# Optimization experiments

Measured on AMD Instinct MI355X. Metric: run time of the kernel, lower is better.

The kernel has to match this reference:

```python
import jax, jax.numpy as jnp
import numpy as np

C = 192  # in_channels
B, S, L = 4, 64, 512  # batch, spatial (patch pixels), seq_len (num patches)


def setup_inputs() -> dict:
    key = jax.random.key(0)
    ks = jax.random.split(key, 6)
    scale_in = 1.0 / np.sqrt(C)
    return {
        "query": jax.random.normal(ks[0], (B, C, S, L), jnp.float32),
        "key": jax.random.normal(ks[1], (B, C, S, L), jnp.float32),
        "value": jax.random.normal(ks[2], (B, C, S, L), jnp.float32),
        "in_proj_weight": jax.random.normal(ks[3], (1 + 2 * C, C, 1, 1), jnp.float32) * scale_in,
        "in_proj_bias": jnp.zeros((1 + 2 * C,), jnp.float32),
        "out_proj_weight": jax.random.normal(ks[4], (C, C, 1, 1), jnp.float32) * scale_in,
        "out_proj_bias": jnp.zeros((C,), jnp.float32),
    }


def reference(query, key, value, in_proj_weight, in_proj_bias, out_proj_weight, out_proj_bias):
    # Separable (linear) attention, MobileViTv2-style.
    c = query.shape[1]
    w = in_proj_weight[:, :, 0, 0]           # (1+2C, C)
    wq, wk, wv = w[:1], w[1:1 + c], w[1 + c:]
    bq, bk, bv = in_proj_bias[:1], in_proj_bias[1:1 + c], in_proj_bias[1 + c:]

    # 1x1 conv projections (pointwise GEMMs over channels)
    q = jnp.einsum('oc,bcsl->bosl', wq, query) + bq[None, :, None, None]   # (B,1,S,L)
    k = jnp.einsum('oc,bcsl->bosl', wk, key) + bk[None, :, None, None]     # (B,C,S,L)
    v = jnp.einsum('oc,bcsl->bosl', wv, value) + bv[None, :, None, None]   # (B,C,S,L)

    # Context scores: softmax over token axis (seq_len); dropout_p=0 (eval)
    context_scores = jax.nn.softmax(q, axis=-1)                            # (B,1,S,L)

    # Weighted context pooling over tokens -> global context per spatial pixel
    context = jnp.sum(k * context_scores, axis=-1, keepdims=True)          # (B,C,S,1)

    # Broadcast multiply with gated value
    out = jax.nn.relu(v) * context                                         # (B,C,S,L)

    # Out projection (1x1 conv)
    wo = out_proj_weight[:, :, 0, 0]
    out = jnp.einsum('oc,bcsl->bosl', wo, out) + out_proj_bias[None, :, None, None]
    return out
```

## Files before the change

kernel.cpp:

```cpp
#include <hip/hip_runtime.h>

#define B_ 4
#define C_ 192
#define S_ 64
#define L_ 512

typedef _Float16 h8 __attribute__((ext_vector_type(8)));
typedef _Float16 h4 __attribute__((ext_vector_type(4)));
typedef _Float16 h2 __attribute__((ext_vector_type(2)));
typedef float f4 __attribute__((ext_vector_type(4)));

__device__ __forceinline__ int swz_l(int l) { return ((l >> 2) ^ l) & 7; }

__global__ __launch_bounds__(512) void k_prep(
    const float* __restrict__ W, const float* __restrict__ Bi,
    const float* __restrict__ Wo, const float* __restrict__ Bo,
    _Float16* __restrict__ wvh, _Float16* __restrict__ woh,
    float* __restrict__ bvf, float* __restrict__ bof)
{
    int n = blockIdx.x * 512 + threadIdx.x;
    if (n < 36864)       wvh[n] = (_Float16)W[37056 + n];
    else if (n < 73728)  woh[n - 36864] = (_Float16)Wo[n - 36864];
    else if (n < 73920)  bvf[n - 73728] = Bi[1 + C_ + (n - 73728)];
    else if (n < 74112)  bof[n - 73920] = Bo[n - 73920];
}

__global__ __launch_bounds__(512) void k1_qsoft(
    const float* __restrict__ Q, const float* __restrict__ W,
    float* __restrict__ pbuf)
{
    __shared__ float sm_wq[C_];
    __shared__ float sm_red[8];
    __shared__ float sm_red2[8];

    const int t = threadIdx.x;
    const int b = blockIdx.x >> 6, s = blockIdx.x & 63;
    const int lane = t & 63, w = t >> 6;

    if (t < C_) sm_wq[t] = W[t];
    __syncthreads();

    const float* qp = Q + ((size_t)(b * C_) * S_ + s) * L_ + t;
    float a0 = 0.f, a1 = 0.f, a2 = 0.f, a3 = 0.f;
    for (int c = 0; c < C_; c += 4) {
        a0 += sm_wq[c + 0] * qp[(size_t)(c + 0) * (S_ * L_)];
        a1 += sm_wq[c + 1] * qp[(size_t)(c + 1) * (S_ * L_)];
        a2 += sm_wq[c + 2] * qp[(size_t)(c + 2) * (S_ * L_)];
        a3 += sm_wq[c + 3] * qp[(size_t)(c + 3) * (S_ * L_)];
    }
    float q = (a0 + a1) + (a2 + a3);

    float m = q;
#pragma unroll
    for (int off = 32; off >= 1; off >>= 1) m = fmaxf(m, __shfl_down(m, off));
    if (lane == 0) sm_red[w] = m;
    __syncthreads();
    float bm = sm_red[0];
#pragma unroll
    for (int i = 1; i < 8; ++i) bm = fmaxf(bm, sm_red[i]);
    float e = __expf(q - bm);
    float sum = e;
#pragma unroll
    for (int off = 32; off >= 1; off >>= 1) sum += __shfl_down(sum, off);
    if (lane == 0) sm_red2[w] = sum;
    __syncthreads();
    float tot = 0.f;
#pragma unroll
    for (int i = 0; i < 8; ++i) tot += sm_red2[i];

    pbuf[(size_t)blockIdx.x * 512 + t] = e / tot;
}

__global__ __launch_bounds__(256) void k2_kbar(
    const float* __restrict__ K, const float* __restrict__ pbuf,
    float* __restrict__ kbar)
{
    const int t = threadIdx.x;
    const int bs = blockIdx.x / 6;
    const int cg = blockIdx.x - bs * 6;
    const int b = bs >> 6, s = bs & 63;
    const int wv = t >> 6, lane = t & 63;

    const f4* pp = (const f4*)(pbuf + (size_t)bs * 512);
    f4 p0 = pp[lane], p1 = pp[lane + 64];

    for (int r = 0; r < 8; ++r) {
        int c = cg * 32 + wv * 8 + r;
        const f4* kp = (const f4*)(K + ((size_t)(b * C_ + c) * S_ + s) * L_);
        f4 x0 = kp[lane], x1 = kp[lane + 64];
        float d = x0[0]*p0[0] + x0[1]*p0[1] + x0[2]*p0[2] + x0[3]*p0[3]
                + x1[0]*p1[0] + x1[1]*p1[1] + x1[2]*p1[2] + x1[3]*p1[3];
#pragma unroll
        for (int off = 32; off >= 1; off >>= 1) d += __shfl_down(d, off);
        if (lane == 0) kbar[(size_t)bs * C_ + c] = d;
    }
}

__global__ __launch_bounds__(192) void k3_ctx(
    const float* __restrict__ W, const float* __restrict__ Bi,
    const float* __restrict__ kbar, float* __restrict__ ctxb)
{
    __shared__ float kb[C_];
    const int t = threadIdx.x, bs = blockIdx.x;
    kb[t] = kbar[(size_t)bs * C_ + t];
    __syncthreads();
    const float* wr = W + (size_t)(1 + t) * C_;
    float a0 = 0.f, a1 = 0.f, a2 = 0.f, a3 = 0.f;
    for (int c = 0; c < C_; c += 4) {
        a0 += wr[c + 0] * kb[c + 0];
        a1 += wr[c + 1] * kb[c + 1];
        a2 += wr[c + 2] * kb[c + 2];
        a3 += wr[c + 3] * kb[c + 3];
    }
    ctxb[(size_t)bs * C_ + t] = (a0 + a1) + (a2 + a3) + Bi[1 + t];
}

__global__ __launch_bounds__(512, 4) void k_main(
    const float* __restrict__ V,
    const _Float16* __restrict__ wvh,
    const _Float16* __restrict__ woh,
    const float* __restrict__ ctxb,
    const float* __restrict__ bvf,
    const float* __restrict__ bof,
    float* __restrict__ Out)
{
    __shared__ __attribute__((aligned(16))) _Float16 sm_v[64 * 192];
    __shared__ __attribute__((aligned(16))) _Float16 sm_u[64 * 192];
    __shared__ __attribute__((aligned(16))) _Float16 sm_w[192 * 40];

    const int t = threadIdx.x;
    const int bs = blockIdx.x >> 3;
    const int chunk = blockIdx.x & 7;
    const int b = bs >> 6, s = bs & 63;
    const int l0 = chunk * 64;
    const int w = t >> 6, lane = t & 63;
    const int quad = lane >> 4, n16 = lane & 15;

    {
        const int tx = t & 15, rp = t >> 4;
        h2* smv2 = (h2*)sm_v;
#pragma unroll
        for (int i = 0; i < 3; ++i) {
            int cp = i * 32 + rp;
            const float* vp = V + ((size_t)(b * C_ + 2 * cp) * S_ + s) * L_ + l0 + tx * 4;
            f4 x0 = *(const f4*)vp;
            f4 x1 = *(const f4*)(vp + S_ * L_);
#pragma unroll
            for (int k = 0; k < 4; ++k) {
                int l = tx * 4 + k;
                int dw = l * 96 + (((cp >> 2) ^ swz_l(l)) << 2) + (cp & 3);
                h2 hh; hh[0] = (_Float16)x0[k]; hh[1] = (_Float16)x1[k];
                smv2[dw] = hh;
            }
        }
    }

    f4 acc[3][2];
#pragma unroll
    for (int i = 0; i < 3; ++i)
#pragma unroll
        for (int j = 0; j < 2; ++j) acc[i][j] = (f4)0.f;

    for (int kt = 0; kt < 6; ++kt) {
        __syncthreads();
        {
            const unsigned int* src = (const unsigned int*)wvh;
            unsigned int* dst = (unsigned int*)sm_w;
#pragma unroll
            for (int i = 0; i < 6; ++i) {
                int d = t + i * 512;
                int r = d >> 4, cd = d & 15;
                dst[r * 20 + cd] = src[r * 96 + kt * 16 + cd];
            }
        }
        __syncthreads();

        h8 bfr[2];
#pragma unroll
        for (int j = 0; j < 2; ++j) {
            int l = (w >> 2) * 32 + j * 16 + n16;
            bfr[j] = *(const h8*)(sm_v + l * 192 + ((((kt * 4 + quad)) ^ swz_l(l)) << 3));
        }
#pragma unroll
        for (int i = 0; i < 3; ++i) {
            int o = (w & 3) * 48 + i * 16 + n16;
            h8 afr = *(const h8*)(sm_w + o * 40 + quad * 8);
#pragma unroll
            for (int j = 0; j < 2; ++j)
                acc[i][j] = __builtin_amdgcn_mfma_f32_16x16x32_f16(afr, bfr[j], acc[i][j], 0, 0, 0);
        }
    }

#pragma unroll
    for (int i = 0; i < 3; ++i) {
        int o0 = (w & 3) * 48 + i * 16 + quad * 4;
        f4 cx = *(const f4*)(ctxb + (size_t)bs * C_ + o0);
        f4 bv = *(const f4*)(bvf + o0);
#pragma unroll
        for (int j = 0; j < 2; ++j) {
            int l = (w >> 2) * 32 + j * 16 + n16;
            h4 uu;
#pragma unroll
            for (int r = 0; r < 4; ++r) {
                float v = acc[i][j][r] + bv[r];
                uu[r] = (_Float16)(fmaxf(v, 0.f) * cx[r]);
            }
            *(h4*)(sm_u + l * 192 + (((o0 >> 3) ^ swz_l(l)) << 3) + (o0 & 7)) = uu;
        }
    }

    f4 acc2[2][3];
#pragma unroll
    for (int i = 0; i < 2; ++i)
#pragma unroll
        for (int j = 0; j < 3; ++j) acc2[i][j] = (f4)0.f;

    for (int kt = 0; kt < 6; ++kt) {
        __syncthreads();
        {
            const unsigned int* src = (const unsigned int*)woh;
            unsigned int* dst = (unsigned int*)sm_w;
#pragma unroll
            for (int i = 0; i < 6; ++i) {
                int d = t + i * 512;
                int r = d >> 4, cd = d & 15;
                dst[r * 20 + cd] = src[r * 96 + kt * 16 + cd];
            }
        }
        __syncthreads();

        h8 afr2[2];
#pragma unroll
        for (int i = 0; i < 2; ++i) {
            int l = (w >> 2) * 32 + i * 16 + n16;
            afr2[i] = *(const h8*)(sm_u + l * 192 + ((((kt * 4 + quad)) ^ swz_l(l)) << 3));
        }
#pragma unroll
        for (int j = 0; j < 3; ++j) {
            int p = (w & 3) * 48 + j * 16 + n16;
            h8 bfr = *(const h8*)(sm_w + p * 40 + quad * 8);
#pragma unroll
            for (int i = 0; i < 2; ++i)
                acc2[i][j] = __builtin_amdgcn_mfma_f32_16x16x32_f16(afr2[i], bfr, acc2[i][j], 0, 0, 0);
        }
    }

#pragma unroll
    for (int j = 0; j < 3; ++j) {
        int p = (w & 3) * 48 + j * 16 + n16;
        float bo = bof[p];
        float* obase = Out + ((size_t)(b * C_ + p) * S_ + s) * L_ + l0;
#pragma unroll
        for (int i = 0; i < 2; ++i) {
            int l = (w >> 2) * 32 + i * 16 + quad * 4;
            f4 ov = acc2[i][j];
            ov[0] += bo; ov[1] += bo; ov[2] += bo; ov[3] += bo;
            *(f4*)(obase + l) = ov;
        }
    }
}

extern "C" void kernel_launch(void* const* d_in, const int* in_sizes, int n_in,
                              void* d_out, int out_size, void* d_ws, size_t ws_size,
                              hipStream_t stream) {
    const float* Q  = (const float*)d_in[0];
    const float* K  = (const float*)d_in[1];
    const float* V  = (const float*)d_in[2];
    const float* W  = (const float*)d_in[3];
    const float* Bi = (const float*)d_in[4];
    const float* Wo = (const float*)d_in[5];
    const float* Bo = (const float*)d_in[6];
    float* Out = (float*)d_out;

    char* ws = (char*)d_ws;
    _Float16* wvh = (_Float16*)(ws);
    _Float16* woh = (_Float16*)(ws + 73728);
    float*    bvf = (float*)(ws + 147456);
    float*    bof = (float*)(ws + 148224);
    float*    pbuf = (float*)(ws + 148992);
    float*    kbar = (float*)(ws + 673280);
    float*    ctxb = (float*)(ws + 869888);

    k_prep  <<<dim3(145),      dim3(512), 0, stream>>>(W, Bi, Wo, Bo, wvh, woh, bvf, bof);
    k1_qsoft<<<dim3(B_ * S_),  dim3(512), 0, stream>>>(Q, W, pbuf);
    k2_kbar <<<dim3(B_*S_*6),  dim3(256), 0, stream>>>(K, pbuf, kbar);
    k3_ctx  <<<dim3(B_ * S_),  dim3(192), 0, stream>>>(W, Bi, kbar, ctxb);
    k_main  <<<dim3(B_*S_*8),  dim3(512), 0, stream>>>(V, wvh, woh, ctxb, bvf, bof, Out);
}
```

Baseline: 355.1 us.

## Split q projection, batch kbar loads, transpose Wk, read weights from global in main

```diff
diff --git a/kernel.cpp b/kernel.cpp
--- a/kernel.cpp
+++ b/kernel.cpp
@@ -16,39 +16,62 @@
     const float* __restrict__ W, const float* __restrict__ Bi,
     const float* __restrict__ Wo, const float* __restrict__ Bo,
     _Float16* __restrict__ wvh, _Float16* __restrict__ woh,
+    float* __restrict__ wkT,
     float* __restrict__ bvf, float* __restrict__ bof)
 {
     int n = blockIdx.x * 512 + threadIdx.x;
-    if (n < 36864)       wvh[n] = (_Float16)W[37056 + n];
-    else if (n < 73728)  woh[n - 36864] = (_Float16)Wo[n - 36864];
-    else if (n < 73920)  bvf[n - 73728] = Bi[1 + C_ + (n - 73728)];
-    else if (n < 74112)  bof[n - 73920] = Bo[n - 73920];
-}
-
-__global__ __launch_bounds__(512) void k1_qsoft(
+    if (n < 36864) {
+        wvh[n] = (_Float16)W[37056 + n];
+    } else if (n < 73728) {
+        woh[n - 36864] = (_Float16)Wo[n - 36864];
+    } else if (n < 110592) {
+        int m = n - 73728;
+        int c = m / C_, o = m - c * C_;
+        wkT[m] = W[(1 + o) * C_ + c];
+    } else if (n < 110784) {
+        bvf[n - 110592] = Bi[1 + C_ + (n - 110592)];
+    } else if (n < 110976) {
+        bof[n - 110784] = Bo[n - 110784];
+    }
+}
+
+__global__ __launch_bounds__(512) void k1a_qpart(
     const float* __restrict__ Q, const float* __restrict__ W,
-    float* __restrict__ pbuf)
-{
-    __shared__ float sm_wq[C_];
+    float* __restrict__ qpart)
+{
+    __shared__ float sm_wq[96];
+    const int t = threadIdx.x;
+    const int half = blockIdx.x & 1;
+    const int bs = blockIdx.x >> 1;
+    const int b = bs >> 6, s = bs & 63;
+
+    if (t < 96) sm_wq[t] = W[half * 96 + t];
+    __syncthreads();
+
+    const float* qp = Q + ((size_t)(b * C_ + half * 96) * S_ + s) * L_ + t;
+    const size_t cs = (size_t)S_ * L_;
+    float a[8];
+#pragma unroll
+    for (int u = 0; u < 8; ++u) a[u] = 0.f;
+    for (int c0 = 0; c0 < 96; c0 += 8) {
+#pragma unroll
+        for (int u = 0; u < 8; ++u)
+            a[u] += sm_wq[c0 + u] * qp[(size_t)(c0 + u) * cs];
+    }
+    float q = ((a[0] + a[1]) + (a[2] + a[3])) + ((a[4] + a[5]) + (a[6] + a[7]));
+    qpart[((size_t)(half * 256 + bs)) * 512 + t] = q;
+}
+
+__global__ __launch_bounds__(512) void k1b_soft(
+    const float* __restrict__ qpart, float* __restrict__ pbuf)
+{
     __shared__ float sm_red[8];
     __shared__ float sm_red2[8];
-
     const int t = threadIdx.x;
-    const int b = blockIdx.x >> 6, s = blockIdx.x & 63;
+    const int bs = blockIdx.x;
     const int lane = t & 63, w = t >> 6;
 
-    if (t < C_) sm_wq[t] = W[t];
-    __syncthreads();
-
-    const float* qp = Q + ((size_t)(b * C_) * S_ + s) * L_ + t;
-    float a0 = 0.f, a1 = 0.f, a2 = 0.f, a3 = 0.f;
-    for (int c = 0; c < C_; c += 4) {
-        a0 += sm_wq[c + 0] * qp[(size_t)(c + 0) * (S_ * L_)];
-        a1 += sm_wq[c + 1] * qp[(size_t)(c + 1) * (S_ * L_)];
-        a2 += sm_wq[c + 2] * qp[(size_t)(c + 2) * (S_ * L_)];
-        a3 += sm_wq[c + 3] * qp[(size_t)(c + 3) * (S_ * L_)];
-    }
-    float q = (a0 + a1) + (a2 + a3);
+    float q = qpart[(size_t)bs * 512 + t] + qpart[(size_t)(256 + bs) * 512 + t];
 
     float m = q;
 #pragma unroll
@@ -68,7 +91,7 @@
 #pragma unroll
     for (int i = 0; i < 8; ++i) tot += sm_red2[i];
 
-    pbuf[(size_t)blockIdx.x * 512 + t] = e / tot;
+    pbuf[(size_t)bs * 512 + t] = e / tot;
 }
 
 __global__ __launch_bounds__(256) void k2_kbar(
@@ -84,35 +107,49 @@
     const f4* pp = (const f4*)(pbuf + (size_t)bs * 512);
     f4 p0 = pp[lane], p1 = pp[lane + 64];
 
+    const int cbase = cg * 32 + wv * 8;
+    f4 x0[8], x1[8];
+#pragma unroll
     for (int r = 0; r < 8; ++r) {
-        int c = cg * 32 + wv * 8 + r;
-        const f4* kp = (const f4*)(K + ((size_t)(b * C_ + c) * S_ + s) * L_);
-        f4 x0 = kp[lane], x1 = kp[lane + 64];
-        float d = x0[0]*p0[0] + x0[1]*p0[1] + x0[2]*p0[2] + x0[3]*p0[3]
-                + x1[0]*p1[0] + x1[1]*p1[1] + x1[2]*p1[2] + x1[3]*p1[3];
-#pragma unroll
-        for (int off = 32; off >= 1; off >>= 1) d += __shfl_down(d, off);
-        if (lane == 0) kbar[(size_t)bs * C_ + c] = d;
+        const f4* kp = (const f4*)(K + ((size_t)(b * C_ + cbase + r) * S_ + s) * L_);
+        x0[r] = kp[lane];
+        x1[r] = kp[lane + 64];
+    }
+    float d[8];
+#pragma unroll
+    for (int r = 0; r < 8; ++r) {
+        d[r] = x0[r][0]*p0[0] + x0[r][1]*p0[1] + x0[r][2]*p0[2] + x0[r][3]*p0[3]
+             + x1[r][0]*p1[0] + x1[r][1]*p1[1] + x1[r][2]*p1[2] + x1[r][3]*p1[3];
+    }
+#pragma unroll
+    for (int off = 32; off >= 1; off >>= 1) {
+#pragma unroll
+        for (int r = 0; r < 8; ++r) d[r] += __shfl_down(d[r], off);
+    }
+    if (lane == 0) {
+#pragma unroll
+        for (int r = 0; r < 8; ++r) kbar[(size_t)bs * C_ + cbase + r] = d[r];
     }
 }
 
 __global__ __launch_bounds__(192) void k3_ctx(
-    const float* __restrict__ W, const float* __restrict__ Bi,
+    const float* __restrict__ wkT, const float* __restrict__ Bi,
     const float* __restrict__ kbar, float* __restrict__ ctxb)
 {
     __shared__ float kb[C_];
     const int t = threadIdx.x, bs = blockIdx.x;
     kb[t] = kbar[(size_t)bs * C_ + t];
     __syncthreads();
-    const float* wr = W + (size_t)(1 + t) * C_;
-    float a0 = 0.f, a1 = 0.f, a2 = 0.f, a3 = 0.f;
-    for (int c = 0; c < C_; c += 4) {
-        a0 += wr[c + 0] * kb[c + 0];
-        a1 += wr[c + 1] * kb[c + 1];
-        a2 += wr[c + 2] * kb[c + 2];
-        a3 += wr[c + 3] * kb[c + 3];
-    }
-    ctxb[(size_t)bs * C_ + t] = (a0 + a1) + (a2 + a3) + Bi[1 + t];
+    float a[8];
+#pragma unroll
+    for (int u = 0; u < 8; ++u) a[u] = 0.f;
+    for (int c0 = 0; c0 < C_; c0 += 8) {
+#pragma unroll
+        for (int u = 0; u < 8; ++u)
+            a[u] += wkT[(size_t)(c0 + u) * C_ + t] * kb[c0 + u];
+    }
+    float v = ((a[0] + a[1]) + (a[2] + a[3])) + ((a[4] + a[5]) + (a[6] + a[7]));
+    ctxb[(size_t)bs * C_ + t] = v + Bi[1 + t];
 }
 
 __global__ __launch_bounds__(512, 4) void k_main(
@@ -126,7 +163,6 @@
 {
     __shared__ __attribute__((aligned(16))) _Float16 sm_v[64 * 192];
     __shared__ __attribute__((aligned(16))) _Float16 sm_u[64 * 192];
-    __shared__ __attribute__((aligned(16))) _Float16 sm_w[192 * 40];
 
     const int t = threadIdx.x;
     const int bs = blockIdx.x >> 3;
@@ -135,6 +171,8 @@
     const int l0 = chunk * 64;
     const int w = t >> 6, lane = t & 63;
     const int quad = lane >> 4, n16 = lane & 15;
+    const int otile = (w & 3) * 48;
+    const int ltile = (w >> 2) * 32;
 
     {
         const int tx = t & 15, rp = t >> 4;
@@ -154,6 +192,7 @@
             }
         }
     }
+    __syncthreads();
 
     f4 acc[3][2];
 #pragma unroll
@@ -161,30 +200,18 @@
 #pragma unroll
         for (int j = 0; j < 2; ++j) acc[i][j] = (f4)0.f;
 
+#pragma unroll
     for (int kt = 0; kt < 6; ++kt) {
-        __syncthreads();
-        {
-            const unsigned int* src = (const unsigned int*)wvh;
-            unsigned int* dst = (unsigned int*)sm_w;
-#pragma unroll
-            for (int i = 0; i < 6; ++i) {
-                int d = t + i * 512;
-                int r = d >> 4, cd = d & 15;
-                dst[r * 20 + cd] = src[r * 96 + kt * 16 + cd];
-            }
-        }
-        __syncthreads();
-
         h8 bfr[2];
 #pragma unroll
         for (int j = 0; j < 2; ++j) {
-            int l = (w >> 2) * 32 + j * 16 + n16;
-            bfr[j] = *(const h8*)(sm_v + l * 192 + ((((kt * 4 + quad)) ^ swz_l(l)) << 3));
+            int l = ltile + j * 16 + n16;
+            bfr[j] = *(const h8*)(sm_v + l * 192 + (((kt * 4 + quad) ^ swz_l(l)) << 3));
         }
 #pragma unroll
         for (int i = 0; i < 3; ++i) {
-            int o = (w & 3) * 48 + i * 16 + n16;
-            h8 afr = *(const h8*)(sm_w + o * 40 + quad * 8);
+            int o = otile + i * 16 + n16;
+            h8 afr = *(const h8*)(wvh + (size_t)o * 192 + kt * 32 + quad * 8);
 #pragma unroll
             for (int j = 0; j < 2; ++j)
                 acc[i][j] = __builtin_amdgcn_mfma_f32_16x16x32_f16(afr, bfr[j], acc[i][j], 0, 0, 0);
@@ -193,12 +220,12 @@
 
 #pragma unroll
     for (int i = 0; i < 3; ++i) {
-        int o0 = (w & 3) * 48 + i * 16 + quad * 4;
+        int o0 = otile + i * 16 + quad * 4;
         f4 cx = *(const f4*)(ctxb + (size_t)bs * C_ + o0);
         f4 bv = *(const f4*)(bvf + o0);
 #pragma unroll
         for (int j = 0; j < 2; ++j) {
-            int l = (w >> 2) * 32 + j * 16 + n16;
+            int l = ltile + j * 16 + n16;
             h4 uu;
 #pragma unroll
             for (int r = 0; r < 4; ++r) {
@@ -208,6 +235,7 @@
             *(h4*)(sm_u + l * 192 + (((o0 >> 3) ^ swz_l(l)) << 3) + (o0 & 7)) = uu;
         }
     }
+    __syncthreads();
 
     f4 acc2[2][3];
 #pragma unroll
@@ -215,30 +243,18 @@
 #pragma unroll
         for (int j = 0; j < 3; ++j) acc2[i][j] = (f4)0.f;
 
+#pragma unroll
     for (int kt = 0; kt < 6; ++kt) {
-        __syncthreads();
-        {
-            const unsigned int* src = (const unsigned int*)woh;
-            unsigned int* dst = (unsigned int*)sm_w;
-#pragma unroll
-            for (int i = 0; i < 6; ++i) {
-                int d = t + i * 512;
-                int r = d >> 4, cd = d & 15;
-                dst[r * 20 + cd] = src[r * 96 + kt * 16 + cd];
-            }
-        }
-        __syncthreads();
-
         h8 afr2[2];
 #pragma unroll
         for (int i = 0; i < 2; ++i) {
-            int l = (w >> 2) * 32 + i * 16 + n16;
-            afr2[i] = *(const h8*)(sm_u + l * 192 + ((((kt * 4 + quad)) ^ swz_l(l)) << 3));
+            int l = ltile + i * 16 + n16;
+            afr2[i] = *(const h8*)(sm_u + l * 192 + (((kt * 4 + quad) ^ swz_l(l)) << 3));
         }
 #pragma unroll
         for (int j = 0; j < 3; ++j) {
-            int p = (w & 3) * 48 + j * 16 + n16;
-            h8 bfr = *(const h8*)(sm_w + p * 40 + quad * 8);
+            int p = otile + j * 16 + n16;
+            h8 bfr = *(const h8*)(woh + (size_t)p * 192 + kt * 32 + quad * 8);
 #pragma unroll
             for (int i = 0; i < 2; ++i)
                 acc2[i][j] = __builtin_amdgcn_mfma_f32_16x16x32_f16(afr2[i], bfr, acc2[i][j], 0, 0, 0);
@@ -247,12 +263,12 @@
 
 #pragma unroll
     for (int j = 0; j < 3; ++j) {
-        int p = (w & 3) * 48 + j * 16 + n16;
+        int p = otile + j * 16 + n16;
         float bo = bof[p];
         float* obase = Out + ((size_t)(b * C_ + p) * S_ + s) * L_ + l0;
 #pragma unroll
         for (int i = 0; i < 2; ++i) {
-            int l = (w >> 2) * 32 + i * 16 + quad * 4;
+            int l = ltile + i * 16 + quad * 4;
             f4 ov = acc2[i][j];
             ov[0] += bo; ov[1] += bo; ov[2] += bo; ov[3] += bo;
             *(f4*)(obase + l) = ov;
@@ -273,17 +289,20 @@
     float* Out = (float*)d_out;
 
     char* ws = (char*)d_ws;
-    _Float16* wvh = (_Float16*)(ws);
-    _Float16* woh = (_Float16*)(ws + 73728);
-    float*    bvf = (float*)(ws + 147456);
-    float*    bof = (float*)(ws + 148224);
-    float*    pbuf = (float*)(ws + 148992);
-    float*    kbar = (float*)(ws + 673280);
-    float*    ctxb = (float*)(ws + 869888);
-
-    k_prep  <<<dim3(145),      dim3(512), 0, stream>>>(W, Bi, Wo, Bo, wvh, woh, bvf, bof);
-    k1_qsoft<<<dim3(B_ * S_),  dim3(512), 0, stream>>>(Q, W, pbuf);
-    k2_kbar <<<dim3(B_*S_*6),  dim3(256), 0, stream>>>(K, pbuf, kbar);
-    k3_ctx  <<<dim3(B_ * S_),  dim3(192), 0, stream>>>(W, Bi, kbar, ctxb);
-    k_main  <<<dim3(B_*S_*8),  dim3(512), 0, stream>>>(V, wvh, woh, ctxb, bvf, bof, Out);
-}
+    _Float16* wvh  = (_Float16*)(ws);
+    _Float16* woh  = (_Float16*)(ws + 73728);
+    float*    wkT  = (float*)(ws + 147456);
+    float*    bvf  = (float*)(ws + 294912);
+    float*    bof  = (float*)(ws + 295680);
+    float*    pbuf = (float*)(ws + 296448);
+    float*    qpart= (float*)(ws + 820736);
+    float*    kbar = (float*)(ws + 1869312);
+    float*    ctxb = (float*)(ws + 2065920);
+
+    k_prep   <<<dim3(217),      dim3(512), 0, stream>>>(W, Bi, Wo, Bo, wvh, woh, wkT, bvf, bof);
+    k1a_qpart<<<dim3(B_*S_*2),  dim3(512), 0, stream>>>(Q, W, qpart);
+    k1b_soft <<<dim3(B_ * S_),  dim3(512), 0, stream>>>(qpart, pbuf);
+    k2_kbar  <<<dim3(B_*S_*6),  dim3(256), 0, stream>>>(K, pbuf, kbar);
+    k3_ctx   <<<dim3(B_ * S_),  dim3(192), 0, stream>>>(wkT, Bi, kbar, ctxb);
+    k_main   <<<dim3(B_*S_*8),  dim3(512), 0, stream>>>(V, wvh, woh, ctxb, bvf, bof, Out);
+}
```

Measured after the change: 383.5 us. 8.0% more time.
